# Optimization experiments

Hardware: AMD Instinct MI355X
Metric: run time of the kernel (lower is better)

The kernel has to match this reference:

```python
import jax, jax.numpy as jnp
import numpy as np

G = 4  # number of groups


def _group_vals(h, shift, Ua, Ua1, Ua2, Ua3):
    # h: [B, H]; Ua: [g, H/g, r]; Ua1/2/3: [g, r, H/g]
    B, H = h.shape
    hg = h.reshape(B, G, H // G)
    if shift:
        # torch index = rotate-left by `shift`: new group j reads old group (j+shift)%g
        hg = jnp.roll(hg, -shift, axis=1)
    t = jnp.einsum('bgd,gdr->bgr', hg, Ua)  # shared low-rank projection
    proj = lambda M: jnp.einsum('bgr,grd->bgd', t, M).reshape(B, H)
    return proj(Ua1), proj(Ua2), proj(Ua3)


def setup_inputs() -> dict:
    key = jax.random.key(0)
    ks = jax.random.split(key, 24)
    B, I, H, wR = 8192, 1024, 1024, 256
    hg = H // G
    r01, r23 = 64, 32
    d = {}
    d['x'] = jax.random.normal(ks[0], (B, I), dtype=jnp.float32)
    d['h'] = jax.random.normal(ks[1], (B, H), dtype=jnp.float32)
    d['W'] = 0.1 * jax.random.normal(ks[2], (I, wR), dtype=jnp.float32)
    d['W1'] = 0.1 * jax.random.normal(ks[3], (wR, H), dtype=jnp.float32)
    d['W2'] = 0.1 * jax.random.normal(ks[4], (wR, H), dtype=jnp.float32)
    d['W3'] = 0.1 * jax.random.normal(ks[5], (wR, H), dtype=jnp.float32)
    d['U'] = 0.1 * jax.random.normal(ks[6], (G, hg, r01), dtype=jnp.float32)
    d['U1'] = 0.1 * jax.random.normal(ks[7], (G, r01, hg), dtype=jnp.float32)
    d['U2'] = 0.1 * jax.random.normal(ks[8], (G, r01, hg), dtype=jnp.float32)
    d['U3'] = 0.1 * jax.random.normal(ks[9], (G, r01, hg), dtype=jnp.float32)
    d['UU'] = 0.1 * jax.random.normal(ks[10], (G, hg, r01), dtype=jnp.float32)
    d['UU1'] = 0.1 * jax.random.normal(ks[11], (G, r01, hg), dtype=jnp.float32)
    d['UU2'] = 0.1 * jax.random.normal(ks[12], (G, r01, hg), dtype=jnp.float32)
    d['UU3'] = 0.1 * jax.random.normal(ks[13], (G, r01, hg), dtype=jnp.float32)
    d['UUU'] = 0.1 * jax.random.normal(ks[14], (G, hg, r23), dtype=jnp.float32)
    d['UUU1'] = 0.1 * jax.random.normal(ks[15], (G, r23, hg), dtype=jnp.float32)
    d['UUU2'] = 0.1 * jax.random.normal(ks[16], (G, r23, hg), dtype=jnp.float32)
    d['UUU3'] = 0.1 * jax.random.normal(ks[17], (G, r23, hg), dtype=jnp.float32)
    d['UUUU'] = 0.1 * jax.random.normal(ks[18], (G, hg, r23), dtype=jnp.float32)
    d['UUUU1'] = 0.1 * jax.random.normal(ks[19], (G, r23, hg), dtype=jnp.float32)
    d['UUUU2'] = 0.1 * jax.random.normal(ks[20], (G, r23, hg), dtype=jnp.float32)
    d['UUUU3'] = 0.1 * jax.random.normal(ks[21], (G, r23, hg), dtype=jnp.float32)
    d['bias_r'] = jnp.ones((1, H), dtype=jnp.float32)
    d['bias_gate'] = jnp.ones((1, H), dtype=jnp.float32)
    d['bias_update'] = jnp.ones((1, H), dtype=jnp.float32)
    return d


def reference(x, h, W, W1, W2, W3, U, U1, U2, U3, UU, UU1, UU2, UU3,
              UUU, UUU1, UUU2, UUU3, UUUU, UUUU1, UUUU2, UUUU3,
              bias_r, bias_gate, bias_update):
    u1, u2, u3 = _group_vals(h, 0, U, U1, U2, U3)
    uu1, uu2, uu3 = _group_vals(h, 1, UU, UU1, UU2, UU3)
    uuu1, uuu2, uuu3 = _group_vals(h, 2, UUU, UUU1, UUU2, UUU3)
    uuuu1, uuuu2, uuuu3 = _group_vals(h, 3, UUUU, UUUU1, UUUU2, UUUU3)
    xw = x @ W  # [B, wRank]
    w1, w2, w3 = xw @ W1, xw @ W2, xw @ W3
    r = jax.nn.sigmoid(w1 + u1 + uu1 + uuu1 + uuuu1 + bias_r)
    z = jax.nn.sigmoid(w2 + u2 + uu2 + uuu2 + uuuu2 + bias_gate)
    c_tilda = jnp.tanh(w3 + r * (u3 + uu3 + uuu3 + uuuu3) + bias_update)
    return z * h + (1.0 - z) * c_tilda
```

## Files before the change

kernel.cpp:

```cpp
#include <hip/hip_runtime.h>

typedef short bf16x8 __attribute__((ext_vector_type(8)));
typedef float f32x4 __attribute__((ext_vector_type(4)));
typedef float f32x16 __attribute__((ext_vector_type(16)));

__device__ __forceinline__ unsigned short f2bf(float f) {
  union { float f; unsigned u; } c; c.f = f;
  unsigned u = c.u;
  u += 0x7FFFu + ((u >> 16) & 1u);
  return (unsigned short)(u >> 16);
}
__device__ __forceinline__ float bf2f(unsigned short h) {
  union { unsigned u; float f; } c; c.u = ((unsigned)h) << 16;
  return c.f;
}
__device__ __forceinline__ void split2(float v, unsigned short& hi, unsigned short& lo) {
  union { float f; unsigned u; } c; c.f = v;
  unsigned uh = c.u & 0xFFFF0000u;
  hi = (unsigned short)(uh >> 16);
  union { unsigned u; float f; } d; d.u = uh;
  lo = f2bf(v - d.f);
}
__device__ __forceinline__ void gload16(const void* g, void* l) {
  __builtin_amdgcn_global_load_lds((const __attribute__((address_space(1))) void*)g,
                                   (__attribute__((address_space(3))) void*)l, 16, 0, 0);
}
__device__ __forceinline__ float sigm(float x) { return 1.0f / (1.0f + __expf(-x)); }
__device__ __forceinline__ float tanha(float x) { return 1.0f - 2.0f / (1.0f + __expf(2.0f * x)); }

__device__ __forceinline__ size_t fragIdxA(int row, int col) {
  int mb = row >> 7, rb = (row >> 5) & 3, l5 = row & 31;
  int cc = col >> 6, k4 = (col >> 4) & 3, hi = (col >> 3) & 1, e = col & 7;
  return ((size_t)(mb * 20 + cc) * 16 + rb * 4 + k4) * 512 + (hi * 32 + l5) * 8 + e;
}

__global__ __launch_bounds__(256) void s123(
    const float* __restrict__ W,
    const float* __restrict__ U, const float* __restrict__ UU,
    const float* __restrict__ UUU, const float* __restrict__ UUUU,
    const float* __restrict__ W1, const float* __restrict__ W2, const float* __restrict__ W3,
    const float* __restrict__ A1, const float* __restrict__ A2, const float* __restrict__ A3,
    const float* __restrict__ B1, const float* __restrict__ B2, const float* __restrict__ B3,
    const float* __restrict__ C1, const float* __restrict__ C2, const float* __restrict__ C3,
    const float* __restrict__ D1, const float* __restrict__ D2, const float* __restrict__ D3,
    unsigned short* __restrict__ Wt, unsigned short* __restrict__ Bg,
    unsigned short* __restrict__ Btp) {
  int gidx = blockIdx.x * 256 + threadIdx.x;
  if (gidx < 262144) {
    int idx = gidx;
    int n = idx >> 10, k = idx & 1023;
    Wt[idx] = f2bf(W[k * 256 + n]);
  } else if (gidx < 458752) {
    int idx = gidx - 262144;
    int g = idx / 49152;
    int rem = idx - g * 49152;
    int n = rem >> 8, k = rem & 255;
    int jj = 0, rr = n;
#pragma unroll
    for (int s = 0; s < 3; ++s) {
      int w = (((g - jj) & 3) < 2) ? 64 : 32;
      if (rr >= w) { rr -= w; ++jj; }
    }
    int v = (g - jj) & 3;
    int rv = (v < 2) ? 64 : 32;
    const float* M = (v == 0) ? U : (v == 1) ? UU : (v == 2) ? UUU : UUUU;
    Bg[idx] = f2bf(M[(jj * 256 + k) * rv + rr]);
  } else {
    int idx = gidx - 458752;
    int blk = idx / 12288;
    int w   = idx - blk * 12288;
    int frag = w >> 9, fl = (w >> 3) & 63, e = w & 7;
    int cb = blk & 3, jk = blk >> 2;
    int kts = jk % 7, j = jk / 7;
    int kt = (kts < 4) ? kts : (kts + 4);
    int q = frag >> 3, colblk = (frag >> 2) & 1, k4 = frag & 3;
    int c  = cb * 64 + colblk * 32 + (fl & 31);
    int k2 = k4 * 16 + (fl >> 5) * 8 + e;
    float val;
    if (kt < 8) {
      int kk = kt * 64 + k2;
      const float* Wp = (q == 0) ? W1 : (q == 1) ? W2 : W3;
      val = Wp[kk * 1024 + j * 256 + c];
    } else {
      int kT = (kt - 8) * 64 + k2;
      int v, r, rv;
      if (kT < 64)       { v = 0; r = kT;       rv = 64; }
      else if (kT < 128) { v = 1; r = kT - 64;  rv = 64; }
      else if (kT < 160) { v = 2; r = kT - 128; rv = 32; }
      else               { v = 3; r = kT - 160; rv = 32; }
      const float* M;
      if (v == 0)      M = (q == 0) ? A1 : (q == 1) ? A2 : A3;
      else if (v == 1) M = (q == 0) ? B1 : (q == 1) ? B2 : B3;
      else if (v == 2) M = (q == 0) ? C1 : (q == 1) ? C2 : C3;
      else             M = (q == 0) ? D1 : (q == 1) ? D2 : D3;
      val = M[(j * rv + r) * 256 + c];
    }
    Btp[idx] = f2bf(val);
  }
}

__device__ __forceinline__ void g1_body(const float* __restrict__ x,
                                        const unsigned short* __restrict__ Wt,
                                        unsigned short* __restrict__ Abuf,
                                        char* lds, int mb, int nb, int tid) {
  const int lane = tid & 63, wid = tid >> 6;
  const int wn = wid;
  f32x4 acc[2][2] = {};
  float4 xr[2];
  const int r0 = tid >> 4, f4c = tid & 15;
  const float* xbase = x + (size_t)(mb * 32) * 1024 + f4c * 4;

  auto loadX = [&](int kt) {
#pragma unroll
    for (int q = 0; q < 2; ++q)
      xr[q] = *(const float4*)(xbase + (size_t)(q * 16 + r0) * 1024 + kt * 64);
  };
  auto writeA = [&](int buf) {
#pragma unroll
    for (int q = 0; q < 2; ++q) {
      int row = q * 16 + r0;
      float4 v = xr[q];
      unsigned short h0, h1, h2, h3, l0, l1, l2, l3;
      split2(v.x, h0, l0); split2(v.y, h1, l1);
      split2(v.z, h2, l2); split2(v.w, h3, l3);
      int ba = row * 128 + ((f4c * 8) ^ ((row & 7) << 4));
      *(uint2*)(lds + buf * 4096 + ba) =
          make_uint2(((unsigned)h1 << 16) | h0, ((unsigned)h3 << 16) | h2);
      *(uint2*)(lds + 8192 + buf * 4096 + ba) =
          make_uint2(((unsigned)l1 << 16) | l0, ((unsigned)l3 << 16) | l2);
    }
  };
  auto stageB = [&](int kt, int buf) {
#pragma unroll
    for (int it = 0; it < 4; ++it) {
      int nloc = it * 32 + wid * 8 + (lane >> 3);
      const char* src = (const char*)Wt + (size_t)(nb * 128 + nloc) * 2048 + kt * 128
                        + (((lane & 7) * 16) ^ ((nloc & 7) << 4));
      gload16(src, lds + 16384 + buf * 16384 + (it * 32 + wid * 8) * 128);
    }
  };

  loadX(0); stageB(0, 0); writeA(0);
  __syncthreads();
#pragma unroll 2
  for (int kt = 0; kt < 16; ++kt) {
    int buf = kt & 1;
    if (kt < 15) {
      loadX(kt + 1); stageB(kt + 1, buf ^ 1);
      asm volatile("s_waitcnt vmcnt(6)" ::: "memory");
    } else {
      asm volatile("s_waitcnt vmcnt(0)" ::: "memory");
    }
    __builtin_amdgcn_s_barrier();
    __builtin_amdgcn_sched_barrier(0);
    const char* hA = lds + buf * 4096;
    const char* lA = lds + 8192 + buf * 4096;
    const char* bB = lds + 16384 + buf * 16384;
#pragma unroll
    for (int ks = 0; ks < 2; ++ks) {
      bf16x8 ah[2], al[2], b[2];
#pragma unroll
      for (int mf = 0; mf < 2; ++mf) {
        int mloc = mf * 16 + (lane & 15);
        int ka = (ks * 64 + (lane >> 4) * 16) ^ ((mloc & 7) << 4);
        ah[mf] = *(const bf16x8*)(hA + mloc * 128 + ka);
        al[mf] = *(const bf16x8*)(lA + mloc * 128 + ka);
      }
#pragma unroll
      for (int nf = 0; nf < 2; ++nf) {
        int nloc = wn * 32 + nf * 16 + (lane & 15);
        int kb = (ks * 64 + (lane >> 4) * 16) ^ ((nloc & 7) << 4);
        b[nf] = *(const bf16x8*)(bB + nloc * 128 + kb);
      }
#pragma unroll
      for (int mf = 0; mf < 2; ++mf)
#pragma unroll
        for (int nf = 0; nf < 2; ++nf) {
          acc[mf][nf] = __builtin_amdgcn_mfma_f32_16x16x32_bf16(ah[mf], b[nf], acc[mf][nf], 0, 0, 0);
          acc[mf][nf] = __builtin_amdgcn_mfma_f32_16x16x32_bf16(al[mf], b[nf], acc[mf][nf], 0, 0, 0);
        }
    }
    if (kt < 15) writeA(buf ^ 1);
    __builtin_amdgcn_sched_barrier(0);
    asm volatile("s_waitcnt lgkmcnt(0)" ::: "memory");
    __builtin_amdgcn_s_barrier();
  }
#pragma unroll
  for (int mf = 0; mf < 2; ++mf)
#pragma unroll
    for (int nf = 0; nf < 2; ++nf)
#pragma unroll
      for (int r = 0; r < 4; ++r) {
        int row = mb * 32 + mf * 16 + (lane >> 4) * 4 + r;
        int col = nb * 128 + wn * 32 + nf * 16 + (lane & 15);
        float val = acc[mf][nf][r];
        unsigned short hi, lo;
        split2(val, hi, lo);
        Abuf[fragIdxA(row, col)] = hi;
        Abuf[fragIdxA(row, col + 256)] = lo;
      }
}

__device__ __forceinline__ void g2_body(const float* __restrict__ h,
                                        const unsigned short* __restrict__ Bg,
                                        unsigned short* __restrict__ Abuf,
                                        char* lds, int mb, int g, int tid) {
  const int lane = tid & 63, wid = tid >> 6;
  const int wm = wid >> 1, wn = wid & 1;
  f32x4 acc[2][6] = {};
  float4 hr[4];
  const int r0 = tid >> 4, f4c = tid & 15;
  const float* hbase = h + (size_t)(mb * 64) * 1024 + g * 256 + f4c * 4;

  auto loadH = [&](int kt) {
#pragma unroll
    for (int q = 0; q < 4; ++q)
      hr[q] = *(const float4*)(hbase + (size_t)(q * 16 + r0) * 1024 + kt * 64);
  };
  auto writeA = [&](int buf) {
#pragma unroll
    for (int q = 0; q < 4; ++q) {
      int row = q * 16 + r0;
      float4 v = hr[q];
      int ba = row * 128 + ((f4c * 8) ^ ((row & 7) << 4));
      *(uint2*)(lds + buf * 8192 + ba) =
          make_uint2(((unsigned)f2bf(v.y) << 16) | f2bf(v.x),
                     ((unsigned)f2bf(v.w) << 16) | f2bf(v.z));
    }
  };
  auto stageB = [&](int kt, int buf) {
#pragma unroll
    for (int it = 0; it < 6; ++it) {
      int nloc = it * 32 + wid * 8 + (lane >> 3);
      const char* src = (const char*)Bg + (size_t)(g * 192 + nloc) * 512 + kt * 128
                        + (((lane & 7) * 16) ^ ((nloc & 7) << 4));
      gload16(src, lds + 16384 + buf * 24576 + (it * 32 + wid * 8) * 128);
    }
  };

  loadH(0); stageB(0, 0); writeA(0);
  __syncthreads();
#pragma unroll
  for (int kt = 0; kt < 4; ++kt) {
    int buf = kt & 1;
    if (kt < 3) { loadH(kt + 1); stageB(kt + 1, buf ^ 1); }
    const char* cA = lds + buf * 8192;
    const char* cB = lds + 16384 + buf * 24576;
#pragma unroll
    for (int ks = 0; ks < 2; ++ks) {
      bf16x8 a[2], b[6];
#pragma unroll
      for (int mf = 0; mf < 2; ++mf) {
        int mloc = wm * 32 + mf * 16 + (lane & 15);
        int ka = (ks * 64 + (lane >> 4) * 16) ^ ((mloc & 7) << 4);
        a[mf] = *(const bf16x8*)(cA + mloc * 128 + ka);
      }
#pragma unroll
      for (int nf = 0; nf < 6; ++nf) {
        int nloc = wn * 96 + nf * 16 + (lane & 15);
        int kb = (ks * 64 + (lane >> 4) * 16) ^ ((nloc & 7) << 4);
        b[nf] = *(const bf16x8*)(cB + nloc * 128 + kb);
      }
#pragma unroll
      for (int mf = 0; mf < 2; ++mf)
#pragma unroll
        for (int nf = 0; nf < 6; ++nf)
          acc[mf][nf] = __builtin_amdgcn_mfma_f32_16x16x32_bf16(a[mf], b[nf], acc[mf][nf], 0, 0, 0);
    }
    if (kt < 3) writeA(buf ^ 1);
    __syncthreads();
  }
#pragma unroll
  for (int mf = 0; mf < 2; ++mf)
#pragma unroll
    for (int nf = 0; nf < 6; ++nf) {
      int n = wn * 96 + nf * 16 + (lane & 15);
      int jj = 0, rr = n;
#pragma unroll
      for (int s = 0; s < 3; ++s) {
        int w = (((g - jj) & 3) < 2) ? 64 : 32;
        if (rr >= w) { rr -= w; ++jj; }
      }
      int v = (g - jj) & 3;
      int offv = (v < 2) ? (v << 6) : (64 + (v << 5));
      int col = 512 + jj * 192 + offv + rr;
#pragma unroll
      for (int r = 0; r < 4; ++r) {
        int row = mb * 64 + wm * 32 + mf * 16 + (lane >> 4) * 4 + r;
        Abuf[fragIdxA(row, col)] = f2bf(acc[mf][nf][r]);
      }
    }
}

__global__ __launch_bounds__(256) void g12(const float* __restrict__ x,
                                           const unsigned short* __restrict__ Wt,
                                           const float* __restrict__ h,
                                           const unsigned short* __restrict__ Bg,
                                           unsigned short* __restrict__ Abuf) {
  __shared__ char lds[65536];
  int b = blockIdx.x, tid = threadIdx.x;
  if (b < 512) {
    g1_body(x, Wt, Abuf, lds, b >> 1, b & 1, tid);
  } else {
    int b2 = b - 512;
    g2_body(h, Bg, Abuf, lds, b2 >> 2, b2 & 3, tid);
  }
}

__global__ __launch_bounds__(256) void g3_main(const unsigned short* __restrict__ Abuf,
                                               const unsigned short* __restrict__ Btp,
                                               const float* __restrict__ h,
                                               const float* __restrict__ bias_r,
                                               const float* __restrict__ bias_g,
                                               const float* __restrict__ bias_u,
                                               float* __restrict__ out) {
  __shared__ char lds[81920];
  const int tid = threadIdx.x, lane = tid & 63, wid = tid >> 6;
  const int flat = blockIdx.x;
  const int xcd = flat & 7, idx = flat >> 3;
  const int mb = xcd * 8 + (idx & 7);
  const int cj = idx >> 3;
  const int cb = cj & 3, j = cj >> 2;
  const int wm = wid >> 1, wn = wid & 1;
  f32x16 acc[2][4] = {};

  const char* AbufB = (const char*)Abuf;
  const char* BtpB  = (const char*)Btp;

  const int A_cc[11]  = {0, 4, 1, 5, 2, 6, 3, 7, 8 + j * 3, 9 + j * 3, 10 + j * 3};
  const int B_kts[11] = {0, 0, 1, 1, 2, 2, 3, 3, 4, 5, 6};
  const bool B_st[11] = {true, false, true, false, true, false, true, false, true, true, true};
  const int B_buf[11] = {0, 0, 1, 1, 0, 0, 1, 1, 0, 1, 0};

  auto stageA = [&](int step, int buf) {
    const char* asrc = AbufB + (size_t)(mb * 20 + A_cc[step]) * 16384 + tid * 16;
#pragma unroll
    for (int it = 0; it < 4; ++it)
      gload16(asrc + it * 4096, lds + buf * 16384 + it * 4096 + wid * 1024);
  };
  auto stageBt = [&](int step, int buf) {
    const char* bsrc = BtpB + (size_t)((j * 7 + B_kts[step]) * 4 + cb) * 24576 + tid * 16;
#pragma unroll
    for (int it = 0; it < 6; ++it)
      gload16(bsrc + it * 4096, lds + 32768 + buf * 24576 + it * 4096 + wid * 1024);
  };

  stageA(0, 0); stageBt(0, 0);
#pragma unroll
  for (int i = 0; i < 11; ++i) {
    const int abuf = i & 1, bbuf = B_buf[i];
    if (i < 10) {
      stageA(i + 1, (i + 1) & 1);
      if (B_st[i + 1]) {
        stageBt(i + 1, B_buf[i + 1]);
        asm volatile("s_waitcnt vmcnt(10)" ::: "memory");
      } else {
        asm volatile("s_waitcnt vmcnt(4)" ::: "memory");
      }
    } else {
      asm volatile("s_waitcnt vmcnt(0)" ::: "memory");
    }
    __builtin_amdgcn_s_barrier();
    __builtin_amdgcn_sched_barrier(0);
    __builtin_amdgcn_s_setprio(1);
    const char* aB = lds + abuf * 16384 + wm * 8192 + lane * 16;
    const char* bB = lds + 32768 + bbuf * 24576 + wn * 4096 + lane * 16;
#pragma unroll
    for (int k4 = 0; k4 < 4; ++k4) {
      bf16x8 a0 = *(const bf16x8*)(aB + k4 * 1024);
      bf16x8 a1 = *(const bf16x8*)(aB + 4096 + k4 * 1024);
#pragma unroll
      for (int q = 0; q < 3; ++q) {
        const int p = (i < 8) ? q : ((q == 2) ? 3 : q);
        bf16x8 b = *(const bf16x8*)(bB + q * 8192 + k4 * 1024);
        acc[0][p] = __builtin_amdgcn_mfma_f32_32x32x16_bf16(a0, b, acc[0][p], 0, 0, 0);
        acc[1][p] = __builtin_amdgcn_mfma_f32_32x32x16_bf16(a1, b, acc[1][p], 0, 0, 0);
      }
    }
    __builtin_amdgcn_s_setprio(0);
    __builtin_amdgcn_sched_barrier(0);
    __builtin_amdgcn_s_barrier();
  }
  int cg = j * 256 + cb * 64 + wn * 32 + (lane & 31);
  float br = bias_r[cg], bg = bias_g[cg], bu = bias_u[cg];
#pragma unroll
  for (int mblk = 0; mblk < 2; ++mblk)
#pragma unroll
    for (int r = 0; r < 16; ++r) {
      int row = mb * 128 + wm * 64 + mblk * 32 + (r & 3) + 8 * (r >> 2) + 4 * (lane >> 5);
      float p0 = acc[mblk][0][r], p1 = acc[mblk][1][r];
      float p2 = acc[mblk][2][r], p3 = acc[mblk][3][r];
      float rr = sigm(p0 + br);
      float zz = sigm(p1 + bg);
      float ct = tanha(p2 + rr * p3 + bu);
      float hv = h[(size_t)row * 1024 + cg];
      out[(size_t)row * 1024 + cg] = zz * hv + (1.0f - zz) * ct;
    }
}

extern "C" void kernel_launch(void* const* d_in, const int* in_sizes, int n_in,
                              void* d_out, int out_size, void* d_ws, size_t ws_size,
                              hipStream_t stream) {
  const float* x   = (const float*)d_in[0];
  const float* h   = (const float*)d_in[1];
  const float* W   = (const float*)d_in[2];
  const float* W1  = (const float*)d_in[3];
  const float* W2  = (const float*)d_in[4];
  const float* W3  = (const float*)d_in[5];
  const float* U   = (const float*)d_in[6];
  const float* U1  = (const float*)d_in[7];
  const float* U2  = (const float*)d_in[8];
  const float* U3  = (const float*)d_in[9];
  const float* UU   = (const float*)d_in[10];
  const float* UU1  = (const float*)d_in[11];
  const float* UU2  = (const float*)d_in[12];
  const float* UU3  = (const float*)d_in[13];
  const float* UUU   = (const float*)d_in[14];
  const float* UUU1  = (const float*)d_in[15];
  const float* UUU2  = (const float*)d_in[16];
  const float* UUU3  = (const float*)d_in[17];
  const float* UUUU   = (const float*)d_in[18];
  const float* UUUU1  = (const float*)d_in[19];
  const float* UUUU2  = (const float*)d_in[20];
  const float* UUUU3  = (const float*)d_in[21];
  const float* bias_r = (const float*)d_in[22];
  const float* bias_g = (const float*)d_in[23];
  const float* bias_u = (const float*)d_in[24];

  char* ws = (char*)d_ws;
  unsigned short* Abuf = (unsigned short*)(ws);
  unsigned short* Wt   = (unsigned short*)(ws + 20971520);
  unsigned short* Bg   = (unsigned short*)(ws + 21495808);
  unsigned short* Btp  = (unsigned short*)(ws + 21889024);
  float* out = (float*)d_out;

  s123<<<7168, 256, 0, stream>>>(W, U, UU, UUU, UUUU,
                                 W1, W2, W3, U1, U2, U3, UU1, UU2, UU3,
                                 UUU1, UUU2, UUU3, UUUU1, UUUU2, UUUU3,
                                 Wt, Bg, Btp);
  g12<<<1024, 256, 0, stream>>>(x, Wt, h, Bg, Abuf);
  g3_main<<<1024, 256, 0, stream>>>(Abuf, Btp, h, bias_r, bias_g, bias_u, out);
}
```

Before: 90.46 us.

## Split K-steps into halves to shrink LDS footprint in g3 GEMM

Reorders the packed A and B fragment layouts so each 64-wide K chunk divides into two contiguous 32-wide halves. The g3 pipeline then runs 22 half-steps with uniform double buffering instead of 11 full steps with an irregular B reuse schedule. LDS per block falls from 80KB to 40KB, which may allow more resident blocks per CU. The trade-off is twice as many barriers per tile, and B tiles that were previously reused across two steps are now reloaded every step.

```diff
diff --git a/kernel.cpp b/kernel.cpp
--- a/kernel.cpp
+++ b/kernel.cpp
@@ -30,8 +30,10 @@
 
 __device__ __forceinline__ size_t fragIdxA(int row, int col) {
   int mb = row >> 7, rb = (row >> 5) & 3, l5 = row & 31;
-  int cc = col >> 6, k4 = (col >> 4) & 3, hi = (col >> 3) & 1, e = col & 7;
-  return ((size_t)(mb * 20 + cc) * 16 + rb * 4 + k4) * 512 + (hi * 32 + l5) * 8 + e;
+  int cc = col >> 6, khalf = (col >> 5) & 1, k4lo = (col >> 4) & 1;
+  int ehi = (col >> 3) & 1, e = col & 7;
+  int frag = khalf * 8 + rb * 2 + k4lo;
+  return ((size_t)(mb * 20 + cc) * 16 + frag) * 512 + (ehi * 32 + l5) * 8 + e;
 }
 
 __global__ __launch_bounds__(256) void s123(
@@ -73,7 +75,9 @@
     int cb = blk & 3, jk = blk >> 2;
     int kts = jk % 7, j = jk / 7;
     int kt = (kts < 4) ? kts : (kts + 4);
-    int q = frag >> 3, colblk = (frag >> 2) & 1, k4 = frag & 3;
+    int khalf = frag / 12, rem2 = frag - khalf * 12;
+    int q = rem2 >> 2, colblk = (rem2 >> 1) & 1, k4lo = rem2 & 1;
+    int k4 = khalf * 2 + k4lo;
     int c  = cb * 64 + colblk * 32 + (fl & 31);
     int k2 = k4 * 16 + (fl >> 5) * 8 + e;
     float val;
@@ -314,7 +318,7 @@
                                                const float* __restrict__ bias_g,
                                                const float* __restrict__ bias_u,
                                                float* __restrict__ out) {
-  __shared__ char lds[81920];
+  __shared__ char lds[40960];
   const int tid = threadIdx.x, lane = tid & 63, wid = tid >> 6;
   const int flat = blockIdx.x;
   const int xcd = flat & 7, idx = flat >> 3;
@@ -329,50 +333,46 @@
 
   const int A_cc[11]  = {0, 4, 1, 5, 2, 6, 3, 7, 8 + j * 3, 9 + j * 3, 10 + j * 3};
   const int B_kts[11] = {0, 0, 1, 1, 2, 2, 3, 3, 4, 5, 6};
-  const bool B_st[11] = {true, false, true, false, true, false, true, false, true, true, true};
-  const int B_buf[11] = {0, 0, 1, 1, 0, 0, 1, 1, 0, 1, 0};
-
-  auto stageA = [&](int step, int buf) {
-    const char* asrc = AbufB + (size_t)(mb * 20 + A_cc[step]) * 16384 + tid * 16;
-#pragma unroll
-    for (int it = 0; it < 4; ++it)
-      gload16(asrc + it * 4096, lds + buf * 16384 + it * 4096 + wid * 1024);
-  };
-  auto stageBt = [&](int step, int buf) {
-    const char* bsrc = BtpB + (size_t)((j * 7 + B_kts[step]) * 4 + cb) * 24576 + tid * 16;
-#pragma unroll
-    for (int it = 0; it < 6; ++it)
-      gload16(bsrc + it * 4096, lds + 32768 + buf * 24576 + it * 4096 + wid * 1024);
-  };
-
-  stageA(0, 0); stageBt(0, 0);
-#pragma unroll
-  for (int i = 0; i < 11; ++i) {
-    const int abuf = i & 1, bbuf = B_buf[i];
-    if (i < 10) {
-      stageA(i + 1, (i + 1) & 1);
-      if (B_st[i + 1]) {
-        stageBt(i + 1, B_buf[i + 1]);
-        asm volatile("s_waitcnt vmcnt(10)" ::: "memory");
-      } else {
-        asm volatile("s_waitcnt vmcnt(4)" ::: "memory");
-      }
+
+  auto stageA = [&](int i, int khalf, int buf) {
+    const char* asrc = AbufB + (size_t)(mb * 20 + A_cc[i]) * 16384 + khalf * 8192 + tid * 16;
+#pragma unroll
+    for (int it = 0; it < 2; ++it)
+      gload16(asrc + it * 4096, lds + buf * 8192 + it * 4096 + wid * 1024);
+  };
+  auto stageBt = [&](int i, int khalf, int buf) {
+    const char* bsrc = BtpB + (size_t)((j * 7 + B_kts[i]) * 4 + cb) * 24576 + khalf * 12288 + tid * 16;
+#pragma unroll
+    for (int it = 0; it < 3; ++it)
+      gload16(bsrc + it * 4096, lds + 16384 + buf * 12288 + it * 4096 + wid * 1024);
+  };
+
+  stageA(0, 0, 0); stageBt(0, 0, 0);
+#pragma unroll
+  for (int s = 0; s < 22; ++s) {
+    const int buf = s & 1;
+    const int i = s >> 1;
+    if (s < 21) {
+      const int sn = s + 1;
+      stageA(sn >> 1, sn & 1, buf ^ 1);
+      stageBt(sn >> 1, sn & 1, buf ^ 1);
+      asm volatile("s_waitcnt vmcnt(5)" ::: "memory");
     } else {
       asm volatile("s_waitcnt vmcnt(0)" ::: "memory");
     }
     __builtin_amdgcn_s_barrier();
     __builtin_amdgcn_sched_barrier(0);
     __builtin_amdgcn_s_setprio(1);
-    const char* aB = lds + abuf * 16384 + wm * 8192 + lane * 16;
-    const char* bB = lds + 32768 + bbuf * 24576 + wn * 4096 + lane * 16;
-#pragma unroll
-    for (int k4 = 0; k4 < 4; ++k4) {
-      bf16x8 a0 = *(const bf16x8*)(aB + k4 * 1024);
-      bf16x8 a1 = *(const bf16x8*)(aB + 4096 + k4 * 1024);
+    const char* aB = lds + buf * 8192 + lane * 16;
+    const char* bB = lds + 16384 + buf * 12288 + wn * 2048 + lane * 16;
+#pragma unroll
+    for (int k4l = 0; k4l < 2; ++k4l) {
+      bf16x8 a0 = *(const bf16x8*)(aB + (wm * 2 + 0) * 2048 + k4l * 1024);
+      bf16x8 a1 = *(const bf16x8*)(aB + (wm * 2 + 1) * 2048 + k4l * 1024);
 #pragma unroll
       for (int q = 0; q < 3; ++q) {
         const int p = (i < 8) ? q : ((q == 2) ? 3 : q);
-        bf16x8 b = *(const bf16x8*)(bB + q * 8192 + k4 * 1024);
+        bf16x8 b = *(const bf16x8*)(bB + q * 4096 + k4l * 1024);
         acc[0][p] = __builtin_amdgcn_mfma_f32_32x32x16_bf16(a0, b, acc[0][p], 0, 0, 0);
         acc[1][p] = __builtin_amdgcn_mfma_f32_32x32x16_bf16(a1, b, acc[1][p], 0, 0, 0);
       }
```

Result: slower. 104.7 us (+15.8%).

## Load A operands directly into MFMA fragment registers, bypassing LDS staging

Applied to the files above, without the earlier changes.

In both the x@W and grouped h-projection GEMM bodies, the fp32 A tiles are now loaded straight from global memory into per-lane registers laid out as MFMA fragments. They are converted (and split into hi/lo bf16 in g1) right before the MFMA calls, so the LDS write/read round trip for A and one barrier/lgkm wait per iteration go away. LDS shrinks to hold only the B tiles, which may allow higher occupancy. The g1 and g2 blocks are also interleaved by block index rather than run as contiguous ranges. The cost is more vector registers for the double-buffered raw fp32 fragments and less coalesced global loads of A.

```diff
diff --git a/kernel.cpp b/kernel.cpp
--- a/kernel.cpp
+++ b/kernel.cpp
@@ -30,8 +30,8 @@
 
 __device__ __forceinline__ size_t fragIdxA(int row, int col) {
   int mb = row >> 7, rb = (row >> 5) & 3, l5 = row & 31;
-  int cc = col >> 6, k4 = (col >> 4) & 3, hi = (col >> 3) & 1, e = col & 7;
-  return ((size_t)(mb * 20 + cc) * 16 + rb * 4 + k4) * 512 + (hi * 32 + l5) * 8 + e;
+  int cc = col >> 6, k4 = (col >> 4) & 3, ehi = (col >> 3) & 1, e = col & 7;
+  return ((size_t)(mb * 20 + cc) * 16 + rb * 4 + k4) * 512 + (ehi * 32 + l5) * 8 + e;
 }
 
 __global__ __launch_bounds__(256) void s123(
@@ -106,29 +106,18 @@
   const int lane = tid & 63, wid = tid >> 6;
   const int wn = wid;
   f32x4 acc[2][2] = {};
-  float4 xr[2];
-  const int r0 = tid >> 4, f4c = tid & 15;
-  const float* xbase = x + (size_t)(mb * 32) * 1024 + f4c * 4;
-
-  auto loadX = [&](int kt) {
-#pragma unroll
-    for (int q = 0; q < 2; ++q)
-      xr[q] = *(const float4*)(xbase + (size_t)(q * 16 + r0) * 1024 + kt * 64);
-  };
-  auto writeA = [&](int buf) {
-#pragma unroll
-    for (int q = 0; q < 2; ++q) {
-      int row = q * 16 + r0;
-      float4 v = xr[q];
-      unsigned short h0, h1, h2, h3, l0, l1, l2, l3;
-      split2(v.x, h0, l0); split2(v.y, h1, l1);
-      split2(v.z, h2, l2); split2(v.w, h3, l3);
-      int ba = row * 128 + ((f4c * 8) ^ ((row & 7) << 4));
-      *(uint2*)(lds + buf * 4096 + ba) =
-          make_uint2(((unsigned)h1 << 16) | h0, ((unsigned)h3 << 16) | h2);
-      *(uint2*)(lds + 8192 + buf * 4096 + ba) =
-          make_uint2(((unsigned)l1 << 16) | l0, ((unsigned)l3 << 16) | l2);
-    }
+  f32x4 araw[2][8];
+  const float* xfrag = x + (size_t)(mb * 32) * 1024 + ((lane >> 4) << 3);
+
+  auto loadA = [&](int kt, int buf) {
+#pragma unroll
+    for (int mf = 0; mf < 2; ++mf)
+#pragma unroll
+      for (int ks = 0; ks < 2; ++ks) {
+        const float* src = xfrag + (size_t)(mf * 16 + (lane & 15)) * 1024 + kt * 64 + ks * 32;
+        araw[buf][(mf * 2 + ks) * 2 + 0] = *(const f32x4*)src;
+        araw[buf][(mf * 2 + ks) * 2 + 1] = *(const f32x4*)(src + 4);
+      }
   };
   auto stageB = [&](int kt, int buf) {
 #pragma unroll
@@ -136,35 +125,41 @@
       int nloc = it * 32 + wid * 8 + (lane >> 3);
       const char* src = (const char*)Wt + (size_t)(nb * 128 + nloc) * 2048 + kt * 128
                         + (((lane & 7) * 16) ^ ((nloc & 7) << 4));
-      gload16(src, lds + 16384 + buf * 16384 + (it * 32 + wid * 8) * 128);
-    }
-  };
-
-  loadX(0); stageB(0, 0); writeA(0);
-  __syncthreads();
+      gload16(src, lds + buf * 16384 + (it * 32 + wid * 8) * 128);
+    }
+  };
+
+  stageB(0, 0); loadA(0, 0);
+  asm volatile("s_waitcnt vmcnt(8)" ::: "memory");
+  __builtin_amdgcn_s_barrier();
 #pragma unroll 2
   for (int kt = 0; kt < 16; ++kt) {
     int buf = kt & 1;
     if (kt < 15) {
-      loadX(kt + 1); stageB(kt + 1, buf ^ 1);
-      asm volatile("s_waitcnt vmcnt(6)" ::: "memory");
+      stageB(kt + 1, buf ^ 1);
+      loadA(kt + 1, buf ^ 1);
+      asm volatile("s_waitcnt vmcnt(12)" ::: "memory");
     } else {
       asm volatile("s_waitcnt vmcnt(0)" ::: "memory");
     }
     __builtin_amdgcn_s_barrier();
     __builtin_amdgcn_sched_barrier(0);
-    const char* hA = lds + buf * 4096;
-    const char* lA = lds + 8192 + buf * 4096;
-    const char* bB = lds + 16384 + buf * 16384;
+    const char* bB = lds + buf * 16384;
 #pragma unroll
     for (int ks = 0; ks < 2; ++ks) {
       bf16x8 ah[2], al[2], b[2];
 #pragma unroll
       for (int mf = 0; mf < 2; ++mf) {
-        int mloc = mf * 16 + (lane & 15);
-        int ka = (ks * 64 + (lane >> 4) * 16) ^ ((mloc & 7) << 4);
-        ah[mf] = *(const bf16x8*)(hA + mloc * 128 + ka);
-        al[mf] = *(const bf16x8*)(lA + mloc * 128 + ka);
+        f32x4 r0 = araw[buf][(mf * 2 + ks) * 2 + 0];
+        f32x4 r1 = araw[buf][(mf * 2 + ks) * 2 + 1];
+#pragma unroll
+        for (int e = 0; e < 4; ++e) {
+          unsigned short hh, ll;
+          split2(r0[e], hh, ll);
+          ah[mf][e] = (short)hh; al[mf][e] = (short)ll;
+          split2(r1[e], hh, ll);
+          ah[mf][4 + e] = (short)hh; al[mf][4 + e] = (short)ll;
+        }
       }
 #pragma unroll
       for (int nf = 0; nf < 2; ++nf) {
@@ -180,9 +175,7 @@
           acc[mf][nf] = __builtin_amdgcn_mfma_f32_16x16x32_bf16(al[mf], b[nf], acc[mf][nf], 0, 0, 0);
         }
     }
-    if (kt < 15) writeA(buf ^ 1);
-    __builtin_amdgcn_sched_barrier(0);
-    asm volatile("s_waitcnt lgkmcnt(0)" ::: "memory");
+    __builtin_amdgcn_sched_barrier(0);
     __builtin_amdgcn_s_barrier();
   }
 #pragma unroll
@@ -208,25 +201,18 @@
   const int lane = tid & 63, wid = tid >> 6;
   const int wm = wid >> 1, wn = wid & 1;
   f32x4 acc[2][6] = {};
-  float4 hr[4];
-  const int r0 = tid >> 4, f4c = tid & 15;
-  const float* hbase = h + (size_t)(mb * 64) * 1024 + g * 256 + f4c * 4;
-
-  auto loadH = [&](int kt) {
-#pragma unroll
-    for (int q = 0; q < 4; ++q)
-      hr[q] = *(const float4*)(hbase + (size_t)(q * 16 + r0) * 1024 + kt * 64);
-  };
-  auto writeA = [&](int buf) {
-#pragma unroll
-    for (int q = 0; q < 4; ++q) {
-      int row = q * 16 + r0;
-      float4 v = hr[q];
-      int ba = row * 128 + ((f4c * 8) ^ ((row & 7) << 4));
-      *(uint2*)(lds + buf * 8192 + ba) =
-          make_uint2(((unsigned)f2bf(v.y) << 16) | f2bf(v.x),
-                     ((unsigned)f2bf(v.w) << 16) | f2bf(v.z));
-    }
+  f32x4 araw[2][8];
+  const float* hfrag = h + (size_t)(mb * 64) * 1024 + g * 256 + ((lane >> 4) << 3);
+
+  auto loadA = [&](int kt, int buf) {
+#pragma unroll
+    for (int mf = 0; mf < 2; ++mf)
+#pragma unroll
+      for (int ks = 0; ks < 2; ++ks) {
+        const float* src = hfrag + (size_t)(wm * 32 + mf * 16 + (lane & 15)) * 1024 + kt * 64 + ks * 32;
+        araw[buf][(mf * 2 + ks) * 2 + 0] = *(const f32x4*)src;
+        araw[buf][(mf * 2 + ks) * 2 + 1] = *(const f32x4*)(src + 4);
+      }
   };
   auto stageB = [&](int kt, int buf) {
 #pragma unroll
@@ -234,26 +220,38 @@
       int nloc = it * 32 + wid * 8 + (lane >> 3);
       const char* src = (const char*)Bg + (size_t)(g * 192 + nloc) * 512 + kt * 128
                         + (((lane & 7) * 16) ^ ((nloc & 7) << 4));
-      gload16(src, lds + 16384 + buf * 24576 + (it * 32 + wid * 8) * 128);
-    }
-  };
-
-  loadH(0); stageB(0, 0); writeA(0);
-  __syncthreads();
+      gload16(src, lds + buf * 24576 + (it * 32 + wid * 8) * 128);
+    }
+  };
+
+  stageB(0, 0); loadA(0, 0);
+  asm volatile("s_waitcnt vmcnt(8)" ::: "memory");
+  __builtin_amdgcn_s_barrier();
 #pragma unroll
   for (int kt = 0; kt < 4; ++kt) {
     int buf = kt & 1;
-    if (kt < 3) { loadH(kt + 1); stageB(kt + 1, buf ^ 1); }
-    const char* cA = lds + buf * 8192;
-    const char* cB = lds + 16384 + buf * 24576;
+    if (kt < 3) {
+      stageB(kt + 1, buf ^ 1);
+      loadA(kt + 1, buf ^ 1);
+      asm volatile("s_waitcnt vmcnt(14)" ::: "memory");
+    } else {
+      asm volatile("s_waitcnt vmcnt(0)" ::: "memory");
+    }
+    __builtin_amdgcn_s_barrier();
+    __builtin_amdgcn_sched_barrier(0);
+    const char* cB = lds + buf * 24576;
 #pragma unroll
     for (int ks = 0; ks < 2; ++ks) {
       bf16x8 a[2], b[6];
 #pragma unroll
       for (int mf = 0; mf < 2; ++mf) {
-        int mloc = wm * 32 + mf * 16 + (lane & 15);
-        int ka = (ks * 64 + (lane >> 4) * 16) ^ ((mloc & 7) << 4);
-        a[mf] = *(const bf16x8*)(cA + mloc * 128 + ka);
+        f32x4 r0 = araw[buf][(mf * 2 + ks) * 2 + 0];
+        f32x4 r1 = araw[buf][(mf * 2 + ks) * 2 + 1];
+#pragma unroll
+        for (int e = 0; e < 4; ++e) {
+          a[mf][e] = (short)f2bf(r0[e]);
+          a[mf][4 + e] = (short)f2bf(r1[e]);
+        }
       }
 #pragma unroll
       for (int nf = 0; nf < 6; ++nf) {
@@ -267,8 +265,8 @@
         for (int nf = 0; nf < 6; ++nf)
           acc[mf][nf] = __builtin_amdgcn_mfma_f32_16x16x32_bf16(a[mf], b[nf], acc[mf][nf], 0, 0, 0);
     }
-    if (kt < 3) writeA(buf ^ 1);
-    __syncthreads();
+    __builtin_amdgcn_sched_barrier(0);
+    __builtin_amdgcn_s_barrier();
   }
 #pragma unroll
   for (int mf = 0; mf < 2; ++mf)
@@ -297,12 +295,13 @@
                                            const float* __restrict__ h,
                                            const unsigned short* __restrict__ Bg,
                                            unsigned short* __restrict__ Abuf) {
-  __shared__ char lds[65536];
+  __shared__ char lds[49152];
   int b = blockIdx.x, tid = threadIdx.x;
-  if (b < 512) {
-    g1_body(x, Wt, Abuf, lds, b >> 1, b & 1, tid);
+  if ((b & 1) == 0) {
+    int b1 = b >> 1;
+    g1_body(x, Wt, Abuf, lds, b1 >> 1, b1 & 1, tid);
   } else {
-    int b2 = b - 512;
+    int b2 = b >> 1;
     g2_body(h, Bg, Abuf, lds, b2 >> 2, b2 & 3, tid);
   }
 }
```

Result: slower. 241.8 us (+167.3%).
